# Performance work log

Hardware: AMD Instinct MI355X
Metric: run time of the kernel (lower is better)

## Reference

```python
import jax, jax.numpy as jnp
import numpy as np

N_NODES = 50000
N_EDGES = 500000
IN_CH = 128
OUT_CH = 256


def setup_inputs() -> dict:
    key = jax.random.key(0)
    k1, k2, k3, k4, k5 = jax.random.split(key, 5)
    x = jax.random.normal(k1, (N_NODES, IN_CH), dtype=jnp.float32)
    edge_index = jax.random.randint(k2, (2, N_EDGES), 0, N_NODES, dtype=jnp.int64)
    edge_weight = jax.random.normal(k3, (N_EDGES,), dtype=jnp.float32)
    # GCNConv linear weight (xavier-uniform) and bias (zeros in torch init; use randn for generality)
    limit = float(np.sqrt(6.0 / (IN_CH + OUT_CH)))
    W = jax.random.uniform(k4, (IN_CH, OUT_CH), minval=-limit, maxval=limit, dtype=jnp.float32)
    b = jnp.zeros((OUT_CH,), dtype=jnp.float32)
    return {"x": x, "W": W, "b": b, "edge_index": edge_index, "edge_weight": edge_weight}


def reference(x, W, b, edge_index, edge_weight):
    N = x.shape[0]
    # GCN wrapper applies sigmoid to edge weights before GCNConv
    ew = jax.nn.sigmoid(edge_weight)
    # gcn_norm: add self-loops with weight 1
    loop = jnp.arange(N, dtype=edge_index.dtype)
    row = jnp.concatenate([edge_index[0], loop])  # source nodes
    col = jnp.concatenate([edge_index[1], loop])  # target nodes
    w = jnp.concatenate([ew, jnp.ones((N,), dtype=x.dtype)])
    # degree on target index, symmetric normalization
    deg = jax.ops.segment_sum(w, col, num_segments=N)
    dinv = jnp.where(deg > 0, jax.lax.rsqrt(deg), jnp.zeros_like(deg))
    norm = dinv[row] * w * dinv[col]  # [E+N]
    # linear transform first (GCNConv: lin has no bias; bias added after aggregation)
    h = x @ W  # [N, OUT_CH]
    msg = h[row] * norm[:, None]  # gather + scale  [E+N, OUT_CH]
    out = jax.ops.segment_sum(msg, col, num_segments=N) + b
    return out
```

## Files before the change

kernel.cpp:

```cpp
#include <hip/hip_runtime.h>
#include <hip/hip_bf16.h>
#include <math.h>

#define NN 50000
#define NE 500000
#define IC 128
#define OC 256
#define NPAD 50176
#define NB 196
#define NEB 1954

typedef short bf16x8 __attribute__((ext_vector_type(8)));
typedef float f32x4 __attribute__((ext_vector_type(4)));

static __device__ inline unsigned short f2b(float f) {
    __hip_bfloat16 h = __float2bfloat16(f);
    return *reinterpret_cast<unsigned short*>(&h);
}
static __device__ inline float b2f(short u) {
    unsigned v = ((unsigned)(unsigned short)u) << 16;
    return __int_as_float(v);
}

__global__ void k_init(unsigned long long* __restrict__ deg64) {
    int i = blockIdx.x * 256 + threadIdx.x;
    deg64[i] = (unsigned long long)(1u << 24);
}

__global__ void k_pass1(const int* __restrict__ col,
                        const float* __restrict__ ew,
                        unsigned long long* __restrict__ deg64,
                        int* __restrict__ eord,
                        const float* __restrict__ x,
                        unsigned short* __restrict__ xb,
                        const float* __restrict__ W,
                        unsigned short* __restrict__ WT) {
    int g = blockIdx.x * 256 + threadIdx.x;
    if (g < NE) {
        int c = col[g];
        float w = 1.0f / (1.0f + expf(-ew[g]));
        unsigned long long pack = (1ull << 32) | (unsigned long long)(unsigned)(w * 16777216.0f);
        unsigned long long old = atomicAdd(&deg64[c], pack);
        eord[g] = (int)(old >> 32);
    }
    const int NX = NN * (IC / 4);
    for (int i = g; i < NX; i += NEB * 256) {
        float4 v = ((const float4*)x)[i];
        ushort4 o;
        o.x = f2b(v.x); o.y = f2b(v.y); o.z = f2b(v.z); o.w = f2b(v.w);
        ((ushort4*)xb)[i] = o;
    }
    if (g < IC * OC) {
        int k = g >> 8;
        int n = g & 255;
        WT[n * IC + k] = f2b(W[g]);
    }
}

__global__ void k_dinv_scan(const unsigned long long* __restrict__ deg64,
                            float* __restrict__ dinv,
                            int* __restrict__ sp,
                            int* __restrict__ bsum) {
    __shared__ int s[256];
    int t = threadIdx.x;
    int i = blockIdx.x * 256 + t;
    unsigned long long v = deg64[i];
    int cnt = (int)(v >> 32);
    float deg = (float)(unsigned)v * (1.0f / 16777216.0f);
    dinv[i] = rsqrtf(deg);
    s[t] = cnt;
    __syncthreads();
    #pragma unroll
    for (int off = 1; off < 256; off <<= 1) {
        int add = (t >= off) ? s[t - off] : 0;
        __syncthreads();
        s[t] += add;
        __syncthreads();
    }
    sp[i] = s[t] - cnt;
    if (t == 255) bsum[blockIdx.x] = s[255];
}

__global__ void k_scan2(int* __restrict__ bsum) {
    __shared__ int s[256];
    int t = threadIdx.x;
    int v = (t < NB) ? bsum[t] : 0;
    s[t] = v;
    __syncthreads();
    #pragma unroll
    for (int off = 1; off < 256; off <<= 1) {
        int add = (t >= off) ? s[t - off] : 0;
        __syncthreads();
        s[t] += add;
        __syncthreads();
    }
    if (t < NB) bsum[t] = s[t] - v;
}

__global__ void k_fill(const int* __restrict__ row,
                       const int* __restrict__ col,
                       const float* __restrict__ ew,
                       const float* __restrict__ dinv,
                       const int* __restrict__ sp,
                       const int* __restrict__ bsum,
                       const int* __restrict__ eord,
                       int2* __restrict__ epack) {
    int e = blockIdx.x * 256 + threadIdx.x;
    if (e < NE) {
        int r = row[e], t = col[e];
        float w = 1.0f / (1.0f + expf(-ew[e]));
        float nrm = dinv[r] * w * dinv[t];
        int pos = sp[t] + bsum[t >> 8] + eord[e];
        int2 p;
        p.x = r;
        p.y = __float_as_int(nrm);
        epack[pos] = p;
    }
}

__global__ __launch_bounds__(256) void k_gather(const unsigned short* __restrict__ xb,
                                                const int* __restrict__ sp,
                                                const int* __restrict__ bsum,
                                                const int2* __restrict__ epack,
                                                const float* __restrict__ dinv,
                                                unsigned short* __restrict__ aggb) {
    int n = blockIdx.x * 16 + (threadIdx.x >> 4);
    if (n >= NN) return;
    int lane = threadIdx.x & 15;
    const bf16x8* xv = (const bf16x8*)xb;

    float di = dinv[n];
    float s2 = di * di;
    bf16x8 xs = xv[(size_t)n * 16 + lane];
    float acc[8];
    #pragma unroll
    for (int c = 0; c < 8; ++c) acc[c] = b2f(xs[c]) * s2;

    int s = sp[n] + bsum[n >> 8];
    int t = sp[n + 1] + bsum[(n + 1) >> 8];
    int e = s;
    for (; e + 2 <= t; e += 2) {
        int2 p0 = epack[e];
        int2 p1 = epack[e + 1];
        bf16x8 v0 = xv[(size_t)p0.x * 16 + lane];
        bf16x8 v1 = xv[(size_t)p1.x * 16 + lane];
        float w0 = __int_as_float(p0.y);
        float w1 = __int_as_float(p1.y);
        #pragma unroll
        for (int c = 0; c < 8; ++c) acc[c] += b2f(v0[c]) * w0;
        #pragma unroll
        for (int c = 0; c < 8; ++c) acc[c] += b2f(v1[c]) * w1;
    }
    if (e < t) {
        int2 p = epack[e];
        bf16x8 v = xv[(size_t)p.x * 16 + lane];
        float w = __int_as_float(p.y);
        #pragma unroll
        for (int c = 0; c < 8; ++c) acc[c] += b2f(v[c]) * w;
    }

    bf16x8 o;
    #pragma unroll
    for (int c = 0; c < 8; ++c) o[c] = (short)f2b(acc[c]);
    ((bf16x8*)aggb)[(size_t)n * 16 + lane] = o;
}

__global__ __launch_bounds__(256) void k_gemm(const unsigned short* __restrict__ agg,
                                              const unsigned short* __restrict__ WT,
                                              const float* __restrict__ bias,
                                              float* __restrict__ out) {
    const int w = threadIdx.x >> 6;
    const int lane = threadIdx.x & 63;
    const int m0 = blockIdx.y * 64 + (w >> 1) * 32;
    const int n0 = blockIdx.x * 128 + (w & 1) * 64;
    const int lm = lane & 15;
    const int lk = (lane >> 4) * 8;

    f32x4 acc[2][4] = {};
    #pragma unroll
    for (int ks = 0; ks < 4; ++ks) {
        const int k0 = ks * 32 + lk;
        bf16x8 wf[4], af[2];
        #pragma unroll
        for (int j = 0; j < 4; ++j)
            wf[j] = *(const bf16x8*)(WT + (size_t)(n0 + j * 16 + lm) * IC + k0);
        #pragma unroll
        for (int i = 0; i < 2; ++i)
            af[i] = *(const bf16x8*)(agg + (size_t)(m0 + i * 16 + lm) * IC + k0);
        #pragma unroll
        for (int i = 0; i < 2; ++i)
            #pragma unroll
            for (int j = 0; j < 4; ++j)
                acc[i][j] = __builtin_amdgcn_mfma_f32_16x16x32_bf16(wf[j], af[i], acc[i][j], 0, 0, 0);
    }

    const int mcol = lane & 15;
    const int nb4 = (lane >> 4) * 4;
    #pragma unroll
    for (int i = 0; i < 2; ++i) {
        int m = m0 + i * 16 + mcol;
        if (m < NN) {
            #pragma unroll
            for (int j = 0; j < 4; ++j) {
                int nn = n0 + j * 16 + nb4;
                float4 bv = *(const float4*)&bias[nn];
                float4 o;
                o.x = acc[i][j][0] + bv.x;
                o.y = acc[i][j][1] + bv.y;
                o.z = acc[i][j][2] + bv.z;
                o.w = acc[i][j][3] + bv.w;
                *(float4*)(out + (size_t)m * OC + nn) = o;
            }
        }
    }
}

extern "C" void kernel_launch(void* const* d_in, const int* in_sizes, int n_in,
                              void* d_out, int out_size, void* d_ws, size_t ws_size,
                              hipStream_t stream) {
    const float* x  = (const float*)d_in[0];
    const float* W  = (const float*)d_in[1];
    const float* b  = (const float*)d_in[2];
    const int*   ei = (const int*)d_in[3];
    const float* ew = (const float*)d_in[4];
    const int* row = ei;
    const int* col = ei + NE;
    float* out = (float*)d_out;

    char* w0 = (char*)d_ws;
    unsigned long long* deg64 = (unsigned long long*)w0;  w0 += NPAD * 8;
    float* dinv  = (float*)w0;                   w0 += NPAD * 4;
    int*   sp    = (int*)w0;                     w0 += NPAD * 4;
    int*   bsum  = (int*)w0;                     w0 += 256 * 4;
    int*   eord  = (int*)w0;                     w0 += NE * 4;
    int2*  epack = (int2*)w0;                    w0 += NE * 8;
    unsigned short* WT   = (unsigned short*)w0;  w0 += IC * OC * 2;
    unsigned short* xb   = (unsigned short*)w0;  w0 += (size_t)NN * IC * 2;
    unsigned short* aggb = (unsigned short*)w0;

    k_init      <<<NB, 256, 0, stream>>>(deg64);
    k_pass1     <<<NEB, 256, 0, stream>>>(col, ew, deg64, eord, x, xb, W, WT);
    k_dinv_scan <<<NB, 256, 0, stream>>>(deg64, dinv, sp, bsum);
    k_scan2     <<<1, 256, 0, stream>>>(bsum);
    k_fill      <<<NEB, 256, 0, stream>>>(row, col, ew, dinv, sp, bsum, eord, epack);
    k_gather    <<<(NN + 15) / 16, 256, 0, stream>>>(xb, sp, bsum, epack, dinv, aggb);
    k_gemm      <<<dim3(2, (NN + 63) / 64), 256, 0, stream>>>(aggb, WT, b, out);
}
```

Baseline: 177.2 us.

## Fuse gather aggregation into GEMM via shared-memory tile and coarsen edge kernels

Merges the per-node neighbor gather and the bf16 MFMA GEMM into one kernel. Each block aggregates 64 nodes into an LDS tile and then multiplies that tile by W, so the aggregated bf16 matrix is never written to or reread from global memory and one launch goes away. Within a node, edges are split across four 16-lane groups and reduced with shuffles. The edge-processing kernels now handle four edges per thread with fewer blocks. The trade-off is less parallelism in the gather phase and possible imbalance across blocks on high-degree nodes.

Result: slower. 227.9 us (+28.6%).

```diff
diff --git a/kernel.cpp b/kernel.cpp
--- a/kernel.cpp
+++ b/kernel.cpp
@@ -8,7 +8,8 @@
 #define OC 256
 #define NPAD 50176
 #define NB 196
-#define NEB 1954
+#define NEB4 489
+#define CONVSTRIDE (NEB4 * 256)
 
 typedef short bf16x8 __attribute__((ext_vector_type(8)));
 typedef float f32x4 __attribute__((ext_vector_type(4)));
@@ -27,7 +28,7 @@
     deg64[i] = (unsigned long long)(1u << 24);
 }
 
-__global__ void k_pass1(const int* __restrict__ col,
+__global__ __launch_bounds__(256) void k_pass1(const int* __restrict__ col,
                         const float* __restrict__ ew,
                         unsigned long long* __restrict__ deg64,
                         int* __restrict__ eord,
@@ -35,16 +36,32 @@
                         unsigned short* __restrict__ xb,
                         const float* __restrict__ W,
                         unsigned short* __restrict__ WT) {
-    int g = blockIdx.x * 256 + threadIdx.x;
-    if (g < NE) {
-        int c = col[g];
-        float w = 1.0f / (1.0f + expf(-ew[g]));
-        unsigned long long pack = (1ull << 32) | (unsigned long long)(unsigned)(w * 16777216.0f);
-        unsigned long long old = atomicAdd(&deg64[c], pack);
-        eord[g] = (int)(old >> 32);
-    }
+    const int base = blockIdx.x * 1024 + threadIdx.x;
+    int   cs[4];
+    float ws[4];
+    #pragma unroll
+    for (int j = 0; j < 4; ++j) {
+        int e = base + j * 256;
+        if (e < NE) { cs[j] = col[e]; ws[j] = ew[e]; }
+    }
+    unsigned long long olds[4];
+    #pragma unroll
+    for (int j = 0; j < 4; ++j) {
+        int e = base + j * 256;
+        if (e < NE) {
+            float w = 1.0f / (1.0f + expf(-ws[j]));
+            unsigned long long pack = (1ull << 32) | (unsigned long long)(unsigned)(w * 16777216.0f);
+            olds[j] = atomicAdd(&deg64[cs[j]], pack);
+        }
+    }
+    #pragma unroll
+    for (int j = 0; j < 4; ++j) {
+        int e = base + j * 256;
+        if (e < NE) eord[e] = (int)(olds[j] >> 32);
+    }
+    const int g = blockIdx.x * 256 + threadIdx.x;
     const int NX = NN * (IC / 4);
-    for (int i = g; i < NX; i += NEB * 256) {
+    for (int i = g; i < NX; i += CONVSTRIDE) {
         float4 v = ((const float4*)x)[i];
         ushort4 o;
         o.x = f2b(v.x); o.y = f2b(v.y); o.z = f2b(v.z); o.w = f2b(v.w);
@@ -97,7 +114,7 @@
     if (t < NB) bsum[t] = s[t] - v;
 }
 
-__global__ void k_fill(const int* __restrict__ row,
+__global__ __launch_bounds__(256) void k_fill(const int* __restrict__ row,
                        const int* __restrict__ col,
                        const float* __restrict__ ew,
                        const float* __restrict__ dinv,
@@ -105,90 +122,102 @@
                        const int* __restrict__ bsum,
                        const int* __restrict__ eord,
                        int2* __restrict__ epack) {
-    int e = blockIdx.x * 256 + threadIdx.x;
-    if (e < NE) {
-        int r = row[e], t = col[e];
-        float w = 1.0f / (1.0f + expf(-ew[e]));
-        float nrm = dinv[r] * w * dinv[t];
-        int pos = sp[t] + bsum[t >> 8] + eord[e];
-        int2 p;
-        p.x = r;
-        p.y = __float_as_int(nrm);
-        epack[pos] = p;
-    }
-}
-
-__global__ __launch_bounds__(256) void k_gather(const unsigned short* __restrict__ xb,
-                                                const int* __restrict__ sp,
-                                                const int* __restrict__ bsum,
-                                                const int2* __restrict__ epack,
-                                                const float* __restrict__ dinv,
-                                                unsigned short* __restrict__ aggb) {
-    int n = blockIdx.x * 16 + (threadIdx.x >> 4);
-    if (n >= NN) return;
-    int lane = threadIdx.x & 15;
-    const bf16x8* xv = (const bf16x8*)xb;
-
-    float di = dinv[n];
-    float s2 = di * di;
-    bf16x8 xs = xv[(size_t)n * 16 + lane];
-    float acc[8];
-    #pragma unroll
-    for (int c = 0; c < 8; ++c) acc[c] = b2f(xs[c]) * s2;
-
-    int s = sp[n] + bsum[n >> 8];
-    int t = sp[n + 1] + bsum[(n + 1) >> 8];
-    int e = s;
-    for (; e + 2 <= t; e += 2) {
-        int2 p0 = epack[e];
-        int2 p1 = epack[e + 1];
-        bf16x8 v0 = xv[(size_t)p0.x * 16 + lane];
-        bf16x8 v1 = xv[(size_t)p1.x * 16 + lane];
-        float w0 = __int_as_float(p0.y);
-        float w1 = __int_as_float(p1.y);
-        #pragma unroll
-        for (int c = 0; c < 8; ++c) acc[c] += b2f(v0[c]) * w0;
-        #pragma unroll
-        for (int c = 0; c < 8; ++c) acc[c] += b2f(v1[c]) * w1;
-    }
-    if (e < t) {
-        int2 p = epack[e];
-        bf16x8 v = xv[(size_t)p.x * 16 + lane];
-        float w = __int_as_float(p.y);
-        #pragma unroll
-        for (int c = 0; c < 8; ++c) acc[c] += b2f(v[c]) * w;
-    }
-
-    bf16x8 o;
-    #pragma unroll
-    for (int c = 0; c < 8; ++c) o[c] = (short)f2b(acc[c]);
-    ((bf16x8*)aggb)[(size_t)n * 16 + lane] = o;
-}
-
-__global__ __launch_bounds__(256) void k_gemm(const unsigned short* __restrict__ agg,
-                                              const unsigned short* __restrict__ WT,
-                                              const float* __restrict__ bias,
-                                              float* __restrict__ out) {
-    const int w = threadIdx.x >> 6;
-    const int lane = threadIdx.x & 63;
-    const int m0 = blockIdx.y * 64 + (w >> 1) * 32;
-    const int n0 = blockIdx.x * 128 + (w & 1) * 64;
+    const int base = blockIdx.x * 1024 + threadIdx.x;
+    #pragma unroll
+    for (int j = 0; j < 4; ++j) {
+        int e = base + j * 256;
+        if (e < NE) {
+            int r = row[e], t = col[e];
+            float w = 1.0f / (1.0f + expf(-ew[e]));
+            float nrm = dinv[r] * w * dinv[t];
+            int pos = sp[t] + bsum[t >> 8] + eord[e];
+            int2 p;
+            p.x = r;
+            p.y = __float_as_int(nrm);
+            epack[pos] = p;
+        }
+    }
+}
+
+__global__ __launch_bounds__(256) void k_gathergemm(const unsigned short* __restrict__ xb,
+                                                    const int* __restrict__ sp,
+                                                    const int* __restrict__ bsum,
+                                                    const int2* __restrict__ epack,
+                                                    const float* __restrict__ dinv,
+                                                    const unsigned short* __restrict__ WT,
+                                                    const float* __restrict__ bias,
+                                                    float* __restrict__ out) {
+    __shared__ unsigned short As[64][IC + 8];
+    __shared__ int   sstart[65];
+    __shared__ float sdinv[64];
+
+    const int tid = threadIdx.x;
+    const int nb = blockIdx.x * 64;
+
+    if (tid < 65) {
+        int n = nb + tid;
+        sstart[tid] = sp[n] + bsum[n >> 8];
+        if (tid < 64) sdinv[tid] = dinv[n];
+    }
+    __syncthreads();
+
+    const int w = tid >> 6;
+    const int lane = tid & 63;
+    const int eg = lane >> 4;
+    const int l16 = lane & 15;
+
+    for (int r = 0; r < 16; ++r) {
+        int local = r * 4 + w;
+        int n = nb + local;
+        float acc[8] = {0.f, 0.f, 0.f, 0.f, 0.f, 0.f, 0.f, 0.f};
+        if (n < NN) {
+            if (eg == 0) {
+                float di = sdinv[local];
+                float s2 = di * di;
+                bf16x8 xs = *(const bf16x8*)(xb + (size_t)n * IC + l16 * 8);
+                #pragma unroll
+                for (int c = 0; c < 8; ++c) acc[c] = b2f(xs[c]) * s2;
+            }
+            int s = sstart[local], t = sstart[local + 1];
+            for (int e = s + eg; e < t; e += 4) {
+                int2 p = epack[e];
+                bf16x8 v = *(const bf16x8*)(xb + (size_t)p.x * IC + l16 * 8);
+                float wg = __int_as_float(p.y);
+                #pragma unroll
+                for (int c = 0; c < 8; ++c) acc[c] += b2f(v[c]) * wg;
+            }
+            #pragma unroll
+            for (int c = 0; c < 8; ++c) {
+                acc[c] += __shfl_xor(acc[c], 16);
+                acc[c] += __shfl_xor(acc[c], 32);
+            }
+        }
+        if (eg == 0) {
+            bf16x8 o;
+            #pragma unroll
+            for (int c = 0; c < 8; ++c) o[c] = (short)f2b(acc[c]);
+            *(bf16x8*)&As[local][l16 * 8] = o;
+        }
+    }
+    __syncthreads();
+
+    const int n0 = w * 64;
     const int lm = lane & 15;
     const int lk = (lane >> 4) * 8;
 
-    f32x4 acc[2][4] = {};
+    f32x4 acc[4][4] = {};
     #pragma unroll
     for (int ks = 0; ks < 4; ++ks) {
         const int k0 = ks * 32 + lk;
-        bf16x8 wf[4], af[2];
+        bf16x8 wf[4], af[4];
         #pragma unroll
         for (int j = 0; j < 4; ++j)
             wf[j] = *(const bf16x8*)(WT + (size_t)(n0 + j * 16 + lm) * IC + k0);
         #pragma unroll
-        for (int i = 0; i < 2; ++i)
-            af[i] = *(const bf16x8*)(agg + (size_t)(m0 + i * 16 + lm) * IC + k0);
+        for (int i = 0; i < 4; ++i)
+            af[i] = *(const bf16x8*)&As[i * 16 + lm][k0];
         #pragma unroll
-        for (int i = 0; i < 2; ++i)
+        for (int i = 0; i < 4; ++i)
             #pragma unroll
             for (int j = 0; j < 4; ++j)
                 acc[i][j] = __builtin_amdgcn_mfma_f32_16x16x32_bf16(wf[j], af[i], acc[i][j], 0, 0, 0);
@@ -197,8 +226,8 @@
     const int mcol = lane & 15;
     const int nb4 = (lane >> 4) * 4;
     #pragma unroll
-    for (int i = 0; i < 2; ++i) {
-        int m = m0 + i * 16 + mcol;
+    for (int i = 0; i < 4; ++i) {
+        int m = nb + i * 16 + mcol;
         if (m < NN) {
             #pragma unroll
             for (int j = 0; j < 4; ++j) {
@@ -234,15 +263,13 @@
     int*   bsum  = (int*)w0;                     w0 += 256 * 4;
     int*   eord  = (int*)w0;                     w0 += NE * 4;
     int2*  epack = (int2*)w0;                    w0 += NE * 8;
-    unsigned short* WT   = (unsigned short*)w0;  w0 += IC * OC * 2;
-    unsigned short* xb   = (unsigned short*)w0;  w0 += (size_t)NN * IC * 2;
-    unsigned short* aggb = (unsigned short*)w0;
+    unsigned short* WT = (unsigned short*)w0;    w0 += IC * OC * 2;
+    unsigned short* xb = (unsigned short*)w0;
 
     k_init      <<<NB, 256, 0, stream>>>(deg64);
-    k_pass1     <<<NEB, 256, 0, stream>>>(col, ew, deg64, eord, x, xb, W, WT);
+    k_pass1     <<<NEB4, 256, 0, stream>>>(col, ew, deg64, eord, x, xb, W, WT);
     k_dinv_scan <<<NB, 256, 0, stream>>>(deg64, dinv, sp, bsum);
     k_scan2     <<<1, 256, 0, stream>>>(bsum);
-    k_fill      <<<NEB, 256, 0, stream>>>(row, col, ew, dinv, sp, bsum, eord, epack);
-    k_gather    <<<(NN + 15) / 16, 256, 0, stream>>>(xb, sp, bsum, epack, dinv, aggb);
-    k_gemm      <<<dim3(2, (NN + 63) / 64), 256, 0, stream>>>(aggb, WT, b, out);
-}
+    k_fill      <<<NEB4, 256, 0, stream>>>(row, col, ew, dinv, sp, bsum, eord, epack);
+    k_gathergemm<<<(NN + 63) / 64, 256, 0, stream>>>(xb, sp, bsum, epack, dinv, WT, b, out);
+}
```
